# Kernel tuning notes

Measured on AMD Instinct MI355X. Metric: run time of the kernel, lower is better.

## Reference

```python
import jax, jax.numpy as jnp
import numpy as np
import math

NEG_INF = -1e9  # keras Softmax masking uses a large negative additive constant

def setup_inputs() -> dict:
    key = jax.random.key(0)
    k1, k2, k3, k4 = jax.random.split(key, 4)
    B, T, C, H = 4, 4096, 1024, 128
    x = jax.random.normal(k1, (B, T, C), dtype=jnp.float32)
    Wq = jax.random.normal(k2, (C, H), dtype=jnp.float32) * (1.0 / math.sqrt(C))
    Wk = jax.random.normal(k3, (C, H), dtype=jnp.float32) * (1.0 / math.sqrt(C))
    Wv = jax.random.normal(k4, (C, H), dtype=jnp.float32) * (1.0 / math.sqrt(C))
    return {"x": x, "Wq": Wq, "Wk": Wk, "Wv": Wv}

def reference(x, Wq, Wk, Wv):
    # x: [B, T, C]; projections are bias-free Dense layers
    B, T, C = x.shape
    q = jnp.einsum('btc,ch->bth', x, Wq)  # [B, T, H]
    k = jnp.einsum('btc,ch->bth', x, Wk)  # [B, T, H]
    v = jnp.einsum('btc,ch->bth', x, Wv)  # [B, T, H]
    # NOTE: original scales by sqrt(C) (the input channel dim), not sqrt(head_size)
    wei = jnp.einsum('bth,bsh->bts', q, k) / math.sqrt(C)  # [B, T, T]
    causal = jnp.tril(jnp.ones((T, T), dtype=bool))
    wei = jnp.where(causal[None, :, :], wei, NEG_INF)
    wei = jax.nn.softmax(wei, axis=-1)
    # dropout is identity at inference
    out = jnp.einsum('bts,bsh->bth', wei, v)  # [B, T, H]
    return out
```

## Files before the change

### kernel.cpp

```cpp
#include <hip/hip_runtime.h>
#include <hip/hip_bf16.h>

typedef __bf16 bf16x8 __attribute__((ext_vector_type(8)));
typedef __bf16 bf16x4 __attribute__((ext_vector_type(4)));
typedef float  f32x4  __attribute__((ext_vector_type(4)));

#define NB 4
#define TT 4096
#define CC 1024
#define HH 128
#define PS 72
#define MNEG -30000.0f

__device__ inline void gload16(const void* g, void* l) {
  __builtin_amdgcn_global_load_lds(
      (const __attribute__((address_space(1))) void*)g,
      (__attribute__((address_space(3))) void*)l, 16, 0, 0);
}

__global__ void detect_dtype(const unsigned int* __restrict__ xw, int* __restrict__ flag) {
  int t = threadIdx.x;
  int cnt = 0;
#pragma unroll
  for (int i = 0; i < 4; ++i) {
    unsigned int w = xw[t + 64 * i];
    int e = (int)((w >> 7) & 0xFFu);
    cnt += (e >= 100 && e <= 135) ? 1 : 0;
  }
  cnt += __shfl_xor(cnt, 1);  cnt += __shfl_xor(cnt, 2);  cnt += __shfl_xor(cnt, 4);
  cnt += __shfl_xor(cnt, 8);  cnt += __shfl_xor(cnt, 16); cnt += __shfl_xor(cnt, 32);
  if (t == 0) *flag = (cnt >= 128) ? 1 : 0;
}

__global__ __launch_bounds__(256) void transpose_w3(
    const void* __restrict__ Wq, const void* __restrict__ Wk,
    const void* __restrict__ Wv, __bf16* __restrict__ Wt,
    const int* __restrict__ flagp) {
  int isbf = *flagp;
  int which = blockIdx.y;
  const void* W = (which == 0) ? Wq : (which == 1) ? Wk : Wv;
  int idx = blockIdx.x * 256 + threadIdx.x;
  int h = idx >> 10, c = idx & 1023;
  __bf16 val;
  if (isbf) val = ((const __bf16*)W)[c * HH + h];
  else      val = (__bf16)(((const float*)W)[c * HH + h]);
  size_t o = (size_t)(c >> 6) * 24576 + (size_t)which * 8192 +
             (size_t)((c >> 3) & 7) * 1024 + (size_t)h * 8 + (c & 7);
  Wt[o] = val;
}

__global__ __launch_bounds__(768) void qkv_proj(
    const void* __restrict__ x, const __bf16* __restrict__ Wt,
    __bf16* __restrict__ q, __bf16* __restrict__ ktl, __bf16* __restrict__ vtl,
    const int* __restrict__ flagp) {
  __shared__ __align__(16) __bf16 XT[2][4096];
  __shared__ __align__(16) __bf16 WTs[2][24576];
  int isbf = *flagp;
  int tid = threadIdx.x, lane = tid & 63, wave = tid >> 6;
  int which = wave >> 2, rowgrp = wave & 3;
  int l16 = lane & 15, quad = lane >> 4;
  int row0 = blockIdx.x * 64;
  f32x4 acc[8] = {};

#define STAGE(ss, b)                                                          \
  for (int i = wave; i < 56; i += 12) {                                       \
    if (i < 8) {                                                              \
      int row = i * 8 + (lane >> 3), g = lane & 7;                            \
      bf16x8 pk;                                                              \
      if (isbf) {                                                             \
        pk = *(const bf16x8*)((const __bf16*)x + (size_t)(row0 + row) * CC +  \
                              (ss) * 64 + g * 8);                             \
      } else {                                                                \
        const float* xf = (const float*)x + (size_t)(row0 + row) * CC +       \
                          (ss) * 64 + g * 8;                                  \
        f32x4 lo = *(const f32x4*)xf;                                         \
        f32x4 hi = *(const f32x4*)(xf + 4);                                   \
        for (int j = 0; j < 4; ++j) { pk[j] = (__bf16)lo[j]; pk[j+4] = (__bf16)hi[j]; } \
      }                                                                       \
      *(bf16x8*)(&XT[b][g * 512 + (row ^ g) * 8]) = pk;                       \
    } else {                                                                  \
      int j = i - 8;                                                          \
      gload16(Wt + (size_t)(ss) * 24576 + j * 512 + lane * 8,                 \
              &WTs[b][j * 512]);                                              \
    }                                                                         \
  }

  STAGE(0, 0);
  for (int s = 0; s < 16; ++s) {
    int cb = s & 1;
    __syncthreads();
    if (s + 1 < 16) { STAGE(s + 1, cb ^ 1); }
#pragma unroll
    for (int t = 0; t < 2; ++t) {
      int g = t * 4 + quad;
      bf16x8 a = *(const bf16x8*)(&XT[cb][g * 512 + ((rowgrp * 16 + l16) ^ g) * 8]);
#pragma unroll
      for (int nt = 0; nt < 8; ++nt) {
        bf16x8 b = *(const bf16x8*)(&WTs[cb][(size_t)which * 8192 + g * 1024 + (nt * 16 + l16) * 8]);
        acc[nt] = __builtin_amdgcn_mfma_f32_16x16x32_bf16(a, b, acc[nt], 0, 0, 0);
      }
    }
  }
#undef STAGE

  int tile = row0 >> 6;
  if (which == 0) {
#pragma unroll
    for (int nt = 0; nt < 8; ++nt)
#pragma unroll
      for (int r = 0; r < 4; ++r) {
        int row = row0 + rowgrp * 16 + quad * 4 + r;
        q[(size_t)row * HH + nt * 16 + l16] = (__bf16)acc[nt][r];
      }
  } else if (which == 1) {
    __bf16* kb = ktl + (size_t)tile * 8192;
#pragma unroll
    for (int nt = 0; nt < 8; ++nt) {
      int h = nt * 16 + l16, g = h >> 3, j = h & 7;
#pragma unroll
      for (int r = 0; r < 4; ++r) {
        int sidx = rowgrp * 16 + quad * 4 + r;
        kb[g * 512 + sidx * 8 + j] = (__bf16)acc[nt][r];
      }
    }
  } else {
    __bf16* vb = vtl + (size_t)tile * 8192;
#pragma unroll
    for (int nt = 0; nt < 8; ++nt) {
      int h = nt * 16 + l16;
      int sb = rowgrp * 16 + quad * 4;
      bf16x4 pk;
#pragma unroll
      for (int r = 0; r < 4; ++r) pk[r] = (__bf16)acc[nt][r];
      *(bf16x4*)(vb + (sb >> 3) * 1024 + h * 8 + (sb & 7)) = pk;
    }
  }
}

__global__ __launch_bounds__(512, 4) void flash_attn(
    const __bf16* __restrict__ q, const __bf16* __restrict__ ktl,
    const __bf16* __restrict__ vtl, void* __restrict__ out,
    const int* __restrict__ flagp) {
  __shared__ __align__(16) __bf16 PL[8][16 * PS];
  __shared__ float CMB[3][32][68];
  __shared__ float CL[3][32];

  int bx = blockIdx.x;
  int batch, qt, rh;
  if (bx < 256) { batch = bx >> 6; qt = bx & 63; rh = 0; }
  else { int j = bx - 256; batch = j >> 6; qt = 63 - (j & 63); rh = 1; }

  int tid = threadIdx.x, lane = tid & 63, wave = tid >> 6;
  int kg = wave >> 1, rowgrp = wave & 1;
  int l16 = lane & 15, quad = lane >> 4;
  int qb = qt * 64;
  int rb = rh * 32 + rowgrp * 16;
  const __bf16* qp  = q   + (size_t)batch * TT * HH;
  const __bf16* ktb = ktl + (size_t)batch * TT * HH;
  const __bf16* vtb = vtl + (size_t)batch * TT * HH;

  bf16x8 qf[4];
  {
    const __bf16* qrow = qp + (size_t)(qb + rb + l16) * HH + quad * 8;
#pragma unroll
    for (int ks = 0; ks < 4; ++ks) qf[ks] = *(const bf16x8*)(qrow + ks * 32);
  }
  bf16x8 onesf;
#pragma unroll
  for (int j = 0; j < 8; ++j) onesf[j] = (l16 == 0) ? (__bf16)1.0f : (__bf16)0.0f;

  f32x4 acc_o[8] = {};
  f32x4 acc_l = {};
  const float SC = 0.0450842200278f;
  const float M0 = 4.0f;
  int qrl = qb + rb + quad * 4;

  for (int jt = kg; jt <= qt; jt += 4) {
    const __bf16* kt  = ktb + (size_t)jt * 8192;
    const __bf16* vt2 = vtb + (size_t)jt * 8192;

    bf16x8 kf[4][4];
#pragma unroll
    for (int ks = 0; ks < 4; ++ks)
#pragma unroll
      for (int kn = 0; kn < 4; ++kn)
        kf[ks][kn] = *(const bf16x8*)(kt + ((4 * ks + quad) * 64 + kn * 16 + l16) * 8);

    f32x4 accs[4] = {};
#pragma unroll
    for (int ks = 0; ks < 4; ++ks)
#pragma unroll
      for (int kn = 0; kn < 4; ++kn)
        accs[kn] = __builtin_amdgcn_mfma_f32_16x16x32_bf16(qf[ks], kf[ks][kn], accs[kn], 0, 0, 0);

    bf16x8 vf[8];
#pragma unroll
    for (int nt = 0; nt < 8; ++nt)
      vf[nt] = *(const bf16x8*)(vt2 + quad * 1024 + (nt * 16 + l16) * 8);

    float pv[4][4];
    if (jt == qt) {
#pragma unroll
      for (int nt = 0; nt < 4; ++nt) {
        int kcol = jt * 64 + nt * 16 + l16;
#pragma unroll
        for (int r = 0; r < 4; ++r) {
          float z = fmaf(accs[nt][r], SC, -M0);
          z = (kcol <= qrl + r) ? z : MNEG;
          pv[nt][r] = exp2f(z);
        }
      }
    } else {
#pragma unroll
      for (int nt = 0; nt < 4; ++nt)
#pragma unroll
        for (int r = 0; r < 4; ++r)
          pv[nt][r] = exp2f(fmaf(accs[nt][r], SC, -M0));
    }

    __bf16* pw = &PL[wave][0];
#pragma unroll
    for (int nt = 0; nt < 4; ++nt)
#pragma unroll
      for (int r = 0; r < 4; ++r)
        pw[(quad * 4 + r) * PS + nt * 16 + l16] = (__bf16)pv[nt][r];

    {
      bf16x8 pa = *(const bf16x8*)(pw + l16 * PS + quad * 8);
      acc_l = __builtin_amdgcn_mfma_f32_16x16x32_bf16(pa, onesf, acc_l, 0, 0, 0);
#pragma unroll
      for (int nt = 0; nt < 8; ++nt)
        acc_o[nt] = __builtin_amdgcn_mfma_f32_16x16x32_bf16(pa, vf[nt], acc_o[nt], 0, 0, 0);
    }
#pragma unroll
    for (int nt = 0; nt < 8; ++nt)
      vf[nt] = *(const bf16x8*)(vt2 + (4 + quad) * 1024 + (nt * 16 + l16) * 8);
    {
      bf16x8 pa = *(const bf16x8*)(pw + l16 * PS + 32 + quad * 8);
      acc_l = __builtin_amdgcn_mfma_f32_16x16x32_bf16(pa, onesf, acc_l, 0, 0, 0);
#pragma unroll
      for (int nt = 0; nt < 8; ++nt)
        acc_o[nt] = __builtin_amdgcn_mfma_f32_16x16x32_bf16(pa, vf[nt], acc_o[nt], 0, 0, 0);
    }
  }

  int rr = rowgrp * 16 + quad * 4;
  if (kg > 0) {
#pragma unroll
    for (int nt = 0; nt < 4; ++nt)
#pragma unroll
      for (int r = 0; r < 4; ++r)
        CMB[kg - 1][rr + r][nt * 16 + l16] = acc_o[nt][r];
    if (l16 == 0) {
#pragma unroll
      for (int r = 0; r < 4; ++r) CL[kg - 1][rr + r] = acc_l[r];
    }
  }
  __syncthreads();
  int isbf = *flagp;
  __bf16* ob = (__bf16*)out + (size_t)batch * TT * HH;
  float*  of = (float*)out  + (size_t)batch * TT * HH;
  float inv[4];
  if (kg == 0) {
#pragma unroll
    for (int r = 0; r < 4; ++r) {
      float lr = __shfl(acc_l[r], lane & 48);
      lr += CL[0][rr + r] + CL[1][rr + r] + CL[2][rr + r];
      inv[r] = 1.f / fmaxf(lr, 1e-30f);
    }
#pragma unroll
    for (int nt = 0; nt < 4; ++nt)
#pragma unroll
      for (int r = 0; r < 4; ++r) {
        int row = qb + rh * 32 + rr + r;
        int col = nt * 16 + l16;
        float val = acc_o[nt][r] + CMB[0][rr + r][col] + CMB[1][rr + r][col] +
                    CMB[2][rr + r][col];
        val *= inv[r];
        size_t idx = (size_t)row * HH + col;
        if (isbf) ob[idx] = (__bf16)val;
        else      of[idx] = val;
      }
  }
  __syncthreads();
  if (kg > 0) {
#pragma unroll
    for (int nt = 4; nt < 8; ++nt)
#pragma unroll
      for (int r = 0; r < 4; ++r)
        CMB[kg - 1][rr + r][(nt - 4) * 16 + l16] = acc_o[nt][r];
  }
  __syncthreads();
  if (kg == 0) {
#pragma unroll
    for (int nt = 4; nt < 8; ++nt)
#pragma unroll
      for (int r = 0; r < 4; ++r) {
        int row = qb + rh * 32 + rr + r;
        int col = nt * 16 + l16;
        int cc = (nt - 4) * 16 + l16;
        float val = acc_o[nt][r] + CMB[0][rr + r][cc] + CMB[1][rr + r][cc] +
                    CMB[2][rr + r][cc];
        val *= inv[r];
        size_t idx = (size_t)row * HH + col;
        if (isbf) ob[idx] = (__bf16)val;
        else      of[idx] = val;
      }
  }
}

extern "C" void kernel_launch(void* const* d_in, const int* in_sizes, int n_in,
                              void* d_out, int out_size, void* d_ws, size_t ws_size,
                              hipStream_t stream) {
  const void* x  = d_in[0];
  const void* Wq = d_in[1];
  const void* Wk = d_in[2];
  const void* Wv = d_in[3];
  char* wsb = (char*)d_ws;
  __bf16* q   = (__bf16*)wsb;
  __bf16* ktl = q   + (size_t)NB * TT * HH;
  __bf16* vtl = ktl + (size_t)NB * TT * HH;
  __bf16* wt  = vtl + (size_t)NB * TT * HH;
  size_t base = (((size_t)(3 * NB * TT * HH + 3 * CC * HH) * 2) + 255) & ~(size_t)255;
  int* flag = (int*)(wsb + base);
  (void)ws_size; (void)in_sizes; (void)n_in; (void)out_size;

  detect_dtype<<<1, 64, 0, stream>>>((const unsigned int*)x, flag);
  transpose_w3<<<dim3(512, 3), 256, 0, stream>>>(Wq, Wk, Wv, wt, flag);
  qkv_proj<<<256, 768, 0, stream>>>(x, wt, q, ktl, vtl, flag);
  flash_attn<<<NB * 64 * 2, 512, 0, stream>>>(q, ktl, vtl, d_out, flag);
}
```

Baseline: 197.3 us.

## Split attention key tiles across six wave groups instead of four

The flash attention block grows from 512 to 768 threads, so six key-group wave pairs stride over key tiles instead of four. The shared combine buffers grow to hold five partial results. Both V fragment halves are now loaded up front rather than interleaved with the MFMAs. The weight transpose index mapping is also swapped so consecutive threads read contiguous source memory. The aim is more parallelism per query tile and better latency hiding, at the cost of more registers for V, more LDS, and a larger final reduction.

```diff
diff --git a/kernel.cpp b/kernel.cpp
--- a/kernel.cpp
+++ b/kernel.cpp
@@ -40,7 +40,7 @@
   int which = blockIdx.y;
   const void* W = (which == 0) ? Wq : (which == 1) ? Wk : Wv;
   int idx = blockIdx.x * 256 + threadIdx.x;
-  int h = idx >> 10, c = idx & 1023;
+  int h = idx & 127, c = idx >> 7;
   __bf16 val;
   if (isbf) val = ((const __bf16*)W)[c * HH + h];
   else      val = (__bf16)(((const float*)W)[c * HH + h]);
@@ -137,13 +137,13 @@
   }
 }
 
-__global__ __launch_bounds__(512, 4) void flash_attn(
+__global__ __launch_bounds__(768, 3) void flash_attn(
     const __bf16* __restrict__ q, const __bf16* __restrict__ ktl,
     const __bf16* __restrict__ vtl, void* __restrict__ out,
     const int* __restrict__ flagp) {
-  __shared__ __align__(16) __bf16 PL[8][16 * PS];
-  __shared__ float CMB[3][32][68];
-  __shared__ float CL[3][32];
+  __shared__ __align__(16) __bf16 PL[12][16 * PS];
+  __shared__ float CMB[5][32][68];
+  __shared__ float CL[5][32];
 
   int bx = blockIdx.x;
   int batch, qt, rh;
@@ -175,7 +175,7 @@
   const float M0 = 4.0f;
   int qrl = qb + rb + quad * 4;
 
-  for (int jt = kg; jt <= qt; jt += 4) {
+  for (int jt = kg; jt <= qt; jt += 6) {
     const __bf16* kt  = ktb + (size_t)jt * 8192;
     const __bf16* vt2 = vtb + (size_t)jt * 8192;
 
@@ -193,10 +193,12 @@
       for (int kn = 0; kn < 4; ++kn)
         accs[kn] = __builtin_amdgcn_mfma_f32_16x16x32_bf16(qf[ks], kf[ks][kn], accs[kn], 0, 0, 0);
 
-    bf16x8 vf[8];
-#pragma unroll
-    for (int nt = 0; nt < 8; ++nt)
-      vf[nt] = *(const bf16x8*)(vt2 + quad * 1024 + (nt * 16 + l16) * 8);
+    bf16x8 vf[2][8];
+#pragma unroll
+    for (int ks2 = 0; ks2 < 2; ++ks2)
+#pragma unroll
+      for (int nt = 0; nt < 8; ++nt)
+        vf[ks2][nt] = *(const bf16x8*)(vt2 + (ks2 * 4 + quad) * 1024 + (nt * 16 + l16) * 8);
 
     float pv[4][4];
     if (jt == qt) {
@@ -225,22 +227,13 @@
       for (int r = 0; r < 4; ++r)
         pw[(quad * 4 + r) * PS + nt * 16 + l16] = (__bf16)pv[nt][r];
 
-    {
-      bf16x8 pa = *(const bf16x8*)(pw + l16 * PS + quad * 8);
+#pragma unroll
+    for (int ks2 = 0; ks2 < 2; ++ks2) {
+      bf16x8 pa = *(const bf16x8*)(pw + l16 * PS + ks2 * 32 + quad * 8);
       acc_l = __builtin_amdgcn_mfma_f32_16x16x32_bf16(pa, onesf, acc_l, 0, 0, 0);
 #pragma unroll
       for (int nt = 0; nt < 8; ++nt)
-        acc_o[nt] = __builtin_amdgcn_mfma_f32_16x16x32_bf16(pa, vf[nt], acc_o[nt], 0, 0, 0);
-    }
-#pragma unroll
-    for (int nt = 0; nt < 8; ++nt)
-      vf[nt] = *(const bf16x8*)(vt2 + (4 + quad) * 1024 + (nt * 16 + l16) * 8);
-    {
-      bf16x8 pa = *(const bf16x8*)(pw + l16 * PS + 32 + quad * 8);
-      acc_l = __builtin_amdgcn_mfma_f32_16x16x32_bf16(pa, onesf, acc_l, 0, 0, 0);
-#pragma unroll
-      for (int nt = 0; nt < 8; ++nt)
-        acc_o[nt] = __builtin_amdgcn_mfma_f32_16x16x32_bf16(pa, vf[nt], acc_o[nt], 0, 0, 0);
+        acc_o[nt] = __builtin_amdgcn_mfma_f32_16x16x32_bf16(pa, vf[ks2][nt], acc_o[nt], 0, 0, 0);
     }
   }
 
@@ -265,7 +258,8 @@
 #pragma unroll
     for (int r = 0; r < 4; ++r) {
       float lr = __shfl(acc_l[r], lane & 48);
-      lr += CL[0][rr + r] + CL[1][rr + r] + CL[2][rr + r];
+#pragma unroll
+      for (int c = 0; c < 5; ++c) lr += CL[c][rr + r];
       inv[r] = 1.f / fmaxf(lr, 1e-30f);
     }
 #pragma unroll
@@ -274,8 +268,9 @@
       for (int r = 0; r < 4; ++r) {
         int row = qb + rh * 32 + rr + r;
         int col = nt * 16 + l16;
-        float val = acc_o[nt][r] + CMB[0][rr + r][col] + CMB[1][rr + r][col] +
-                    CMB[2][rr + r][col];
+        float val = acc_o[nt][r];
+#pragma unroll
+        for (int c = 0; c < 5; ++c) val += CMB[c][rr + r][col];
         val *= inv[r];
         size_t idx = (size_t)row * HH + col;
         if (isbf) ob[idx] = (__bf16)val;
@@ -299,8 +294,9 @@
         int row = qb + rh * 32 + rr + r;
         int col = nt * 16 + l16;
         int cc = (nt - 4) * 16 + l16;
-        float val = acc_o[nt][r] + CMB[0][rr + r][cc] + CMB[1][rr + r][cc] +
-                    CMB[2][rr + r][cc];
+        float val = acc_o[nt][r];
+#pragma unroll
+        for (int c = 0; c < 5; ++c) val += CMB[c][rr + r][cc];
         val *= inv[r];
         size_t idx = (size_t)row * HH + col;
         if (isbf) ob[idx] = (__bf16)val;
@@ -328,5 +324,5 @@
   detect_dtype<<<1, 64, 0, stream>>>((const unsigned int*)x, flag);
   transpose_w3<<<dim3(512, 3), 256, 0, stream>>>(Wq, Wk, Wv, wt, flag);
   qkv_proj<<<256, 768, 0, stream>>>(x, wt, q, ktl, vtl, flag);
-  flash_attn<<<NB * 64 * 2, 512, 0, stream>>>(q, ktl, vtl, d_out, flag);
-}
+  flash_attn<<<NB * 64 * 2, 768, 0, stream>>>(q, ktl, vtl, d_out, flag);
+}
```

After: 189.6 us. 3.9% less time.
